# Kernel optimization log

Hardware: AMD Instinct MI355X
Metric: run time of the kernel (lower is better)

The kernel has to match this reference:

```python
import jax, jax.numpy as jnp
from jax import lax
import numpy as np

SNN_STEPS = 15
BETA = 0.9
THR = 1.0
SLOPE = 25.0  # snntorch fast_sigmoid default slope

@jax.custom_vjp
def spike(x):
    return (x > 0).astype(x.dtype)

def _spike_fwd(x):
    return (x > 0).astype(x.dtype), x

def _spike_bwd(x, g):
    return (g / (SLOPE * jnp.abs(x) + 1.0) ** 2,)

spike.defvjp(_spike_fwd, _spike_bwd)


def setup_inputs() -> dict:
    key = jax.random.key(0)
    ks = jax.random.split(key, 16)
    B, C, H, S, A, Hd, Rh = 256, 20, 10, 64, 16, 128, 64

    def w(k, shape):
        fan_in = shape[0]
        return jax.random.normal(k, shape, jnp.float32) / jnp.sqrt(jnp.float32(fan_in))

    return {
        "current_state": jax.random.normal(ks[0], (B, S), jnp.float32),
        "actions": jax.random.normal(ks[1], (C, B, H, A), jnp.float32),
        "noise": jax.random.normal(ks[2], (C, B, H, S), jnp.float32),
        "Wse": w(ks[3], (S, Hd)), "bse": jnp.zeros((Hd,), jnp.float32),
        "Wae": w(ks[4], (A, Hd)), "bae": jnp.zeros((Hd,), jnp.float32),
        "W1": w(ks[5], (2 * Hd, Hd)), "b1": jnp.zeros((Hd,), jnp.float32),
        "W2": w(ks[6], (Hd, Hd)), "b2": jnp.zeros((Hd,), jnp.float32),
        "Wdec": w(ks[7], (Hd, S)), "bdec": jnp.zeros((S,), jnp.float32),
        "Wunc": w(ks[8], (Hd, S)), "bunc": jnp.zeros((S,), jnp.float32),
        "Wr1": w(ks[9], (S + A, Rh)), "br1": jnp.zeros((Rh,), jnp.float32),
        "Wr2": w(ks[10], (Rh, Rh)), "br2": jnp.zeros((Rh,), jnp.float32),
        "Wr3": w(ks[11], (Rh, 1)), "br3": jnp.zeros((1,), jnp.float32),
    }


def _plan(current_state, actions, noise, Wse, bse, Wae, bae, W1, b1, W2, b2,
          Wdec, bdec, Wunc, bunc, Wr1, br1, Wr2, br2, Wr3, br3):
    C, B, H, A = actions.shape
    S = current_state.shape[-1]
    CB = C * B
    # fold candidates into batch -> fully vectorized Monte Carlo rollouts
    state0 = jnp.broadcast_to(current_state[None], (C, B, S)).reshape(CB, S)
    acts = actions.transpose(2, 0, 1, 3).reshape(H, CB, A)   # [H, CB, A]
    noi = noise.transpose(2, 0, 1, 3).reshape(H, CB, S)      # [H, CB, S]

    def world_step(state, act_t, noise_t):
        se = jax.nn.relu(state @ Wse + bse)
        ae = jax.nn.relu(act_t @ Wae + bae)
        cur = jnp.concatenate([se, ae], axis=-1) @ W1 + b1   # constant over snn steps

        def snn_step(carry, _):
            mem1, mem2 = carry
            # snntorch Leaky (reset-by-subtraction, reset uses previous spike)
            mem1 = BETA * mem1 + cur - THR * spike(mem1 - THR)
            spk1 = spike(mem1 - THR)
            cur2 = spk1 @ W2 + b2
            mem2 = BETA * mem2 + cur2 - THR * spike(mem2 - THR)
            return (mem1, mem2), None

        zeros = jnp.zeros_like(cur)
        (_, mem2), _ = lax.scan(snn_step, (zeros, zeros), None, length=SNN_STEPS)
        mean = mem2 @ Wdec + bdec
        var = jax.nn.softplus(mem2 @ Wunc + bunc)
        return mean + noise_t * jnp.sqrt(var + 1e-8)  # sample_next_state

    def rollout(state, xs):
        act_t, noise_t = xs
        ns = world_step(state, act_t, noise_t)
        return ns, ns

    _, states = lax.scan(rollout, state0, (acts, noi))       # [H, CB, S]

    # reward model over all (state, action) pairs at once
    x = jnp.concatenate([states, acts], axis=-1)             # [H, CB, S+A]
    h = jax.nn.relu(x @ Wr1 + br1)
    h = jax.nn.relu(h @ Wr2 + br2)
    r = (h @ Wr3 + br3)[..., 0]                              # [H, CB]
    cum = r.sum(axis=0).reshape(C, B).T                      # [B, C]

    best_idx = jnp.argmax(cum, axis=1)                       # [B]
    best_value = jnp.take_along_axis(cum, best_idx[:, None], axis=1)[:, 0]
    best_actions = actions[best_idx, jnp.arange(B)]          # [B, H, A]
    return best_actions, best_value


def reference(current_state, actions, noise, Wse, bse, Wae, bae, W1, b1, W2, b2,
              Wdec, bdec, Wunc, bunc, Wr1, br1, Wr2, br2, Wr3, br3):
    return _plan(current_state, actions, noise, Wse, bse, Wae, bae, W1, b1, W2, b2,
                 Wdec, bdec, Wunc, bunc, Wr1, br1, Wr2, br2, Wr3, br3)


if __name__ == "__main__":
    out = reference(**setup_inputs())
    print(out[0].shape, out[1].shape)
```

## Files before the change

kernel.cpp:

```cpp
#include <hip/hip_runtime.h>
#include <math.h>

#define CC 20
#define BB 256
#define HH 10
#define SS 64
#define AA 16
#define HD 128
#define RH 64
#define CBR (CC*BB)
#define NSNN 15
#define RT 4

__device__ __forceinline__ float softplus_np(float u) {
    if (u > 0.0f) {
        float ef = (float)exp((double)(-u));
        float l1 = (float)log1p((double)ef);
        return __fadd_rn(u, l1);
    } else if (u < 0.0f) {
        float ef = (float)exp((double)u);
        return (float)log1p((double)ef);
    } else {
        return 0.69314718055994530942f;
    }
}

__global__ __launch_bounds__(256, 4) void world_kernel(
    int h,
    const float* __restrict__ current_state,
    const float* __restrict__ actions,
    const float* __restrict__ noise,
    const float* __restrict__ Wse, const float* __restrict__ bse,
    const float* __restrict__ Wae, const float* __restrict__ bae,
    const float* __restrict__ W1,  const float* __restrict__ b1,
    const float* __restrict__ W2,  const float* __restrict__ b2,
    const float* __restrict__ Wdec, const float* __restrict__ bdec,
    const float* __restrict__ Wunc, const float* __restrict__ bunc,
    const float* __restrict__ Wr1, const float* __restrict__ br1,
    const float* __restrict__ Wr2, const float* __restrict__ br2,
    const float* __restrict__ Wr3, const float* __restrict__ br3,
    float* __restrict__ states,
    float* __restrict__ cum)
{
    const int r    = threadIdx.x >> 6;
    const int lane = threadIdx.x & 63;
    const int cb   = blockIdx.x * RT + r;

    __shared__ float s_state[RT][SS];
    __shared__ float s_sae[RT][2*HD];
    __shared__ float s_mem2[RT][HD];
    __shared__ float s_x[RT][SS + AA];
    __shared__ float s_h[RT][RH];
    __shared__ float s_h2[RT][RH];

    s_state[r][lane] = (h == 0) ? current_state[(size_t)(cb % BB)*SS + lane]
                                : states[((size_t)(h-1)*CBR + cb)*SS + lane];

    float a0 = 0.0f, a1 = 0.0f;
    {
        const float* p = Wse + lane;
        for (int i = 0; i < SS; i++) {
            float st = s_state[r][i];
            a0 = fmaf(st, p[i*HD],      a0);
            a1 = fmaf(st, p[i*HD + 64], a1);
        }
    }
    float se0 = fmaxf(__fadd_rn(a0, bse[lane]),      0.0f);
    float se1 = fmaxf(__fadd_rn(a1, bse[64 + lane]), 0.0f);

    const float* act = actions + ((size_t)cb*HH + h)*AA;
    float e0 = 0.0f, e1 = 0.0f;
    {
        const float* p = Wae + lane;
        for (int i = 0; i < AA; i++) {
            float av = act[i];
            e0 = fmaf(av, p[i*HD],      e0);
            e1 = fmaf(av, p[i*HD + 64], e1);
        }
    }
    float ae0 = fmaxf(__fadd_rn(e0, bae[lane]),      0.0f);
    float ae1 = fmaxf(__fadd_rn(e1, bae[64 + lane]), 0.0f);

    s_sae[r][lane]            = se0;
    s_sae[r][64 + lane]       = se1;
    s_sae[r][HD + lane]       = ae0;
    s_sae[r][HD + 64 + lane]  = ae1;

    float c0 = 0.0f, c1 = 0.0f;
    {
        const float* p = W1 + lane;
        for (int i = 0; i < 2*HD; i++) {
            float v = s_sae[r][i];
            c0 = fmaf(v, p[i*HD],      c0);
            c1 = fmaf(v, p[i*HD + 64], c1);
        }
    }
    const float cur0 = __fadd_rn(c0, b1[lane]);
    const float cur1 = __fadd_rn(c1, b1[64 + lane]);

    unsigned mask0 = 0u, mask1 = 0u;
    {
        float m1a = 0.0f, m1b = 0.0f;
        #pragma unroll
        for (int t = 0; t < NSNN; t++) {
            float spa = (__fsub_rn(m1a, 1.0f) > 0.0f) ? 1.0f : 0.0f;
            m1a = __fsub_rn(__fadd_rn(__fmul_rn(0.9f, m1a), cur0), spa);
            if (__fsub_rn(m1a, 1.0f) > 0.0f) mask0 |= (1u << t);
            float spb = (__fsub_rn(m1b, 1.0f) > 0.0f) ? 1.0f : 0.0f;
            m1b = __fsub_rn(__fadd_rn(__fmul_rn(0.9f, m1b), cur1), spb);
            if (__fsub_rn(m1b, 1.0f) > 0.0f) mask1 |= (1u << t);
        }
    }

    float c2a[NSNN], c2b[NSNN];
    #pragma unroll
    for (int t = 0; t < NSNN; t++) { c2a[t] = 0.0f; c2b[t] = 0.0f; }

    const float* W2j = W2 + lane;
    #pragma unroll 1
    for (int k = 0; k < 64; k++) {
        unsigned m = (unsigned)__builtin_amdgcn_readlane((int)mask0, k);
        if (m == 0u) continue;
        const float* p = W2j + (size_t)k * HD;
        float wa = p[0];
        float wb = p[64];
        #pragma unroll
        for (int t = 0; t < NSNN; t++) {
            float sv = __uint_as_float(((m >> t) & 1u) * 0x3f800000u);
            c2a[t] = fmaf(sv, wa, c2a[t]);
            c2b[t] = fmaf(sv, wb, c2b[t]);
        }
    }
    #pragma unroll 1
    for (int k = 0; k < 64; k++) {
        unsigned m = (unsigned)__builtin_amdgcn_readlane((int)mask1, k);
        if (m == 0u) continue;
        const float* p = W2j + (size_t)(64 + k) * HD;
        float wa = p[0];
        float wb = p[64];
        #pragma unroll
        for (int t = 0; t < NSNN; t++) {
            float sv = __uint_as_float(((m >> t) & 1u) * 0x3f800000u);
            c2a[t] = fmaf(sv, wa, c2a[t]);
            c2b[t] = fmaf(sv, wb, c2b[t]);
        }
    }

    {
        const float b2a = b2[lane], b2b = b2[64 + lane];
        float m2a = 0.0f, m2b = 0.0f;
        #pragma unroll
        for (int t = 0; t < NSNN; t++) {
            float ca = __fadd_rn(c2a[t], b2a);
            float spa = (__fsub_rn(m2a, 1.0f) > 0.0f) ? 1.0f : 0.0f;
            m2a = __fsub_rn(__fadd_rn(__fmul_rn(0.9f, m2a), ca), spa);
            float cbv = __fadd_rn(c2b[t], b2b);
            float spb = (__fsub_rn(m2b, 1.0f) > 0.0f) ? 1.0f : 0.0f;
            m2b = __fsub_rn(__fadd_rn(__fmul_rn(0.9f, m2b), cbv), spb);
        }
        s_mem2[r][lane]      = m2a;
        s_mem2[r][64 + lane] = m2b;
    }

    float dm = 0.0f, du = 0.0f;
    {
        const float* pd = Wdec + lane;
        const float* pu = Wunc + lane;
        for (int n = 0; n < HD; n++) {
            float mv = s_mem2[r][n];
            dm = fmaf(mv, pd[n*SS], dm);
            du = fmaf(mv, pu[n*SS], du);
        }
    }
    float mean = __fadd_rn(dm, bdec[lane]);
    float u    = __fadd_rn(du, bunc[lane]);

    float var = softplus_np(u);
    float sv  = sqrtf(__fadd_rn(var, 1e-8f));
    float nz  = noise[((size_t)cb*HH + h)*SS + lane];
    float ns  = __fadd_rn(mean, __fmul_rn(nz, sv));
    states[((size_t)h*CBR + cb)*SS + lane] = ns;

    s_x[r][lane] = ns;
    if (lane < AA) s_x[r][SS + lane] = act[lane];

    float ra = 0.0f;
    for (int i = 0; i < SS + AA; i++)
        ra = fmaf(s_x[r][i], Wr1[i*RH + lane], ra);
    s_h[r][lane] = fmaxf(__fadd_rn(ra, br1[lane]), 0.0f);

    float rg = 0.0f;
    for (int i = 0; i < RH; i++)
        rg = fmaf(s_h[r][i], Wr2[i*RH + lane], rg);
    s_h2[r][lane] = fmaxf(__fadd_rn(rg, br2[lane]), 0.0f);

    float rr = 0.0f;
    for (int k = 0; k < RH; k++)
        rr = fmaf(s_h2[r][k], Wr3[k], rr);
    rr = __fadd_rn(rr, br3[0]);
    if (lane == 0)
        cum[cb] = (h == 0) ? rr : __fadd_rn(cum[cb], rr);
}

__global__ __launch_bounds__(64) void select_kernel(
    const float* __restrict__ cum,
    const float* __restrict__ actions,
    float* __restrict__ out)
{
    const int b = blockIdx.x;
    const int j = threadIdx.x;
    __shared__ int s_c;

    if (j == 0) {
        float best = cum[b];
        int bc = 0;
        for (int c = 1; c < CC; c++) {
            float v = cum[(size_t)c*BB + b];
            if (v > best) { best = v; bc = c; }
        }
        s_c = bc;
        out[(size_t)BB*HH*AA + b] = best;
    }
    __syncthreads();
    const int bc = s_c;
    const float* src = actions + ((size_t)bc*BB + b)*HH*AA;
    for (int i = j; i < HH*AA; i += 64) out[(size_t)b*HH*AA + i] = src[i];
}

extern "C" void kernel_launch(void* const* d_in, const int* in_sizes, int n_in,
                              void* d_out, int out_size, void* d_ws, size_t ws_size,
                              hipStream_t stream)
{
    const float* current_state = (const float*)d_in[0];
    const float* actions = (const float*)d_in[1];
    const float* noise   = (const float*)d_in[2];
    const float* Wse = (const float*)d_in[3];
    const float* bse = (const float*)d_in[4];
    const float* Wae = (const float*)d_in[5];
    const float* bae = (const float*)d_in[6];
    const float* W1  = (const float*)d_in[7];
    const float* b1  = (const float*)d_in[8];
    const float* W2  = (const float*)d_in[9];
    const float* b2  = (const float*)d_in[10];
    const float* Wdec = (const float*)d_in[11];
    const float* bdec = (const float*)d_in[12];
    const float* Wunc = (const float*)d_in[13];
    const float* bunc = (const float*)d_in[14];
    const float* Wr1 = (const float*)d_in[15];
    const float* br1 = (const float*)d_in[16];
    const float* Wr2 = (const float*)d_in[17];
    const float* br2 = (const float*)d_in[18];
    const float* Wr3 = (const float*)d_in[19];
    const float* br3 = (const float*)d_in[20];

    float* states = (float*)d_ws;
    float* cum    = states + (size_t)HH*CBR*SS;

    for (int h = 0; h < HH; h++) {
        world_kernel<<<CBR/RT, RT*64, 0, stream>>>(h, current_state, actions, noise,
            Wse, bse, Wae, bae, W1, b1, W2, b2, Wdec, bdec, Wunc, bunc,
            Wr1, br1, Wr2, br2, Wr3, br3, states, cum);
    }
    select_kernel<<<BB, 64, 0, stream>>>(cum, actions, (float*)d_out);
}
```

Measured before the change: 744.0 us.

## Assign interleaved hidden pairs per lane and vectorize weight loads as float2

Each lane now owns hidden units 2*lane and 2*lane+1 instead of lane and lane+64, so weight and bias reads for Wse, Wae, W1 and W2 become single float2 loads. The two spike-sparse W2 loops are merged into one loop that reads both lanes' masks per iteration and skips a row only when both are empty. The intent is fewer global load instructions and less loop overhead in the world-model step. The spike mask ordering now maps to interleaved W2 rows, which the code handles consistently with the new lane mapping.

```diff
diff --git a/kernel.cpp b/kernel.cpp
--- a/kernel.cpp
+++ b/kernel.cpp
@@ -45,6 +45,7 @@
     const int r    = threadIdx.x >> 6;
     const int lane = threadIdx.x & 63;
     const int cb   = blockIdx.x * RT + r;
+    const int u2   = 2 * lane;
 
     __shared__ float s_state[RT][SS];
     __shared__ float s_sae[RT][2*HD];
@@ -58,45 +59,49 @@
 
     float a0 = 0.0f, a1 = 0.0f;
     {
-        const float* p = Wse + lane;
+        const float* p = Wse + u2;
         for (int i = 0; i < SS; i++) {
             float st = s_state[r][i];
-            a0 = fmaf(st, p[i*HD],      a0);
-            a1 = fmaf(st, p[i*HD + 64], a1);
-        }
-    }
-    float se0 = fmaxf(__fadd_rn(a0, bse[lane]),      0.0f);
-    float se1 = fmaxf(__fadd_rn(a1, bse[64 + lane]), 0.0f);
+            float2 w = *(const float2*)(p + i*HD);
+            a0 = fmaf(st, w.x, a0);
+            a1 = fmaf(st, w.y, a1);
+        }
+    }
+    float2 bsev = *(const float2*)(bse + u2);
+    float se0 = fmaxf(__fadd_rn(a0, bsev.x), 0.0f);
+    float se1 = fmaxf(__fadd_rn(a1, bsev.y), 0.0f);
 
     const float* act = actions + ((size_t)cb*HH + h)*AA;
     float e0 = 0.0f, e1 = 0.0f;
     {
-        const float* p = Wae + lane;
+        const float* p = Wae + u2;
         for (int i = 0; i < AA; i++) {
             float av = act[i];
-            e0 = fmaf(av, p[i*HD],      e0);
-            e1 = fmaf(av, p[i*HD + 64], e1);
-        }
-    }
-    float ae0 = fmaxf(__fadd_rn(e0, bae[lane]),      0.0f);
-    float ae1 = fmaxf(__fadd_rn(e1, bae[64 + lane]), 0.0f);
-
-    s_sae[r][lane]            = se0;
-    s_sae[r][64 + lane]       = se1;
-    s_sae[r][HD + lane]       = ae0;
-    s_sae[r][HD + 64 + lane]  = ae1;
+            float2 w = *(const float2*)(p + i*HD);
+            e0 = fmaf(av, w.x, e0);
+            e1 = fmaf(av, w.y, e1);
+        }
+    }
+    float2 baev = *(const float2*)(bae + u2);
+    float ae0 = fmaxf(__fadd_rn(e0, baev.x), 0.0f);
+    float ae1 = fmaxf(__fadd_rn(e1, baev.y), 0.0f);
+
+    *(float2*)&s_sae[r][u2]      = make_float2(se0, se1);
+    *(float2*)&s_sae[r][HD + u2] = make_float2(ae0, ae1);
 
     float c0 = 0.0f, c1 = 0.0f;
     {
-        const float* p = W1 + lane;
+        const float* p = W1 + u2;
         for (int i = 0; i < 2*HD; i++) {
             float v = s_sae[r][i];
-            c0 = fmaf(v, p[i*HD],      c0);
-            c1 = fmaf(v, p[i*HD + 64], c1);
-        }
-    }
-    const float cur0 = __fadd_rn(c0, b1[lane]);
-    const float cur1 = __fadd_rn(c1, b1[64 + lane]);
+            float2 w = *(const float2*)(p + i*HD);
+            c0 = fmaf(v, w.x, c0);
+            c1 = fmaf(v, w.y, c1);
+        }
+    }
+    float2 b1v = *(const float2*)(b1 + u2);
+    const float cur0 = __fadd_rn(c0, b1v.x);
+    const float cur1 = __fadd_rn(c1, b1v.y);
 
     unsigned mask0 = 0u, mask1 = 0u;
     {
@@ -116,50 +121,45 @@
     #pragma unroll
     for (int t = 0; t < NSNN; t++) { c2a[t] = 0.0f; c2b[t] = 0.0f; }
 
-    const float* W2j = W2 + lane;
+    const float* W2j = W2 + u2;
     #pragma unroll 1
-    for (int k = 0; k < 64; k++) {
-        unsigned m = (unsigned)__builtin_amdgcn_readlane((int)mask0, k);
-        if (m == 0u) continue;
-        const float* p = W2j + (size_t)k * HD;
-        float wa = p[0];
-        float wb = p[64];
-        #pragma unroll
-        for (int t = 0; t < NSNN; t++) {
-            float sv = __uint_as_float(((m >> t) & 1u) * 0x3f800000u);
-            c2a[t] = fmaf(sv, wa, c2a[t]);
-            c2b[t] = fmaf(sv, wb, c2b[t]);
-        }
-    }
-    #pragma unroll 1
-    for (int k = 0; k < 64; k++) {
-        unsigned m = (unsigned)__builtin_amdgcn_readlane((int)mask1, k);
-        if (m == 0u) continue;
-        const float* p = W2j + (size_t)(64 + k) * HD;
-        float wa = p[0];
-        float wb = p[64];
-        #pragma unroll
-        for (int t = 0; t < NSNN; t++) {
-            float sv = __uint_as_float(((m >> t) & 1u) * 0x3f800000u);
-            c2a[t] = fmaf(sv, wa, c2a[t]);
-            c2b[t] = fmaf(sv, wb, c2b[t]);
-        }
-    }
-
-    {
-        const float b2a = b2[lane], b2b = b2[64 + lane];
+    for (int kk = 0; kk < 64; kk++) {
+        unsigned me = (unsigned)__builtin_amdgcn_readlane((int)mask0, kk);
+        unsigned mo = (unsigned)__builtin_amdgcn_readlane((int)mask1, kk);
+        if ((me | mo) == 0u) continue;
+        if (me) {
+            float2 w = *(const float2*)(W2j + (size_t)(2*kk) * HD);
+            #pragma unroll
+            for (int t = 0; t < NSNN; t++) {
+                float sv = __uint_as_float(((me >> t) & 1u) * 0x3f800000u);
+                c2a[t] = fmaf(sv, w.x, c2a[t]);
+                c2b[t] = fmaf(sv, w.y, c2b[t]);
+            }
+        }
+        if (mo) {
+            float2 w = *(const float2*)(W2j + (size_t)(2*kk + 1) * HD);
+            #pragma unroll
+            for (int t = 0; t < NSNN; t++) {
+                float sv = __uint_as_float(((mo >> t) & 1u) * 0x3f800000u);
+                c2a[t] = fmaf(sv, w.x, c2a[t]);
+                c2b[t] = fmaf(sv, w.y, c2b[t]);
+            }
+        }
+    }
+
+    {
+        float2 b2v = *(const float2*)(b2 + u2);
         float m2a = 0.0f, m2b = 0.0f;
         #pragma unroll
         for (int t = 0; t < NSNN; t++) {
-            float ca = __fadd_rn(c2a[t], b2a);
+            float ca = __fadd_rn(c2a[t], b2v.x);
             float spa = (__fsub_rn(m2a, 1.0f) > 0.0f) ? 1.0f : 0.0f;
             m2a = __fsub_rn(__fadd_rn(__fmul_rn(0.9f, m2a), ca), spa);
-            float cbv = __fadd_rn(c2b[t], b2b);
+            float cbv = __fadd_rn(c2b[t], b2v.y);
             float spb = (__fsub_rn(m2b, 1.0f) > 0.0f) ? 1.0f : 0.0f;
             m2b = __fsub_rn(__fadd_rn(__fmul_rn(0.9f, m2b), cbv), spb);
         }
-        s_mem2[r][lane]      = m2a;
-        s_mem2[r][64 + lane] = m2b;
+        *(float2*)&s_mem2[r][u2] = make_float2(m2a, m2b);
     }
 
     float dm = 0.0f, du = 0.0f;
```

Measured after the change: 971.1 us. 1.31x slower.
